# Kernel tuning notes

Hardware: AMD Instinct MI355X
Metric: run time of the kernel (lower is better)

## Reference

```python
import jax, jax.numpy as jnp
import numpy as np

C, H, W = 32, 64, 64
KH, KW = 5, 5
OH, OW = 60, 60
N_IN = C * H * W
B, S = 64, 4096
CAP = 128


def _build_indices():
    # Enumerate every (c, kh, kw, oh, ow) slot of the unfold, matching
    # fold(unfold(order)) in the torch module (stride 1, pad 0, dilation 1).
    c = np.arange(C)[:, None, None, None, None]
    kh = np.arange(KH)[None, :, None, None, None]
    kw = np.arange(KW)[None, None, :, None, None]
    oh = np.arange(OH)[None, None, None, :, None]
    ow = np.arange(OW)[None, None, None, None, :]
    ids = c * (H * W) + (oh + kh) * W + (ow + kw)          # input flat id feeding slot
    ckk = c * (KH * KW) + kh * KW + kw                     # kernel-local channel index
    j = ckk * (OH * OW) + oh * OW + ow                     # flat slot in order_convoled
    ids, j = np.broadcast_arrays(ids, j)
    ids = ids.ravel().astype(np.int64)
    j = j.ravel().astype(np.int64)
    perm = np.argsort(ids, kind='stable')
    sid, sj = ids[perm], j[perm]
    counts = np.bincount(ids, minlength=N_IN)
    Lmax = int(counts.max())                               # = 25 here
    starts = np.concatenate([[0], np.cumsum(counts)[:-1]])
    rank = np.arange(sid.shape[0]) - starts[sid]
    indices = np.full((N_IN, Lmax), -1, dtype=np.int32)
    indices[sid, rank] = sj
    return indices


def setup_inputs() -> dict:
    key = jax.random.key(0)
    spikes = jax.random.randint(key, (B, S, 1, 1), 0, N_IN, dtype=jnp.int32)
    indices = jnp.asarray(_build_indices())
    return {"spikes": spikes, "indices": indices, "out_h": OH, "out_w": OW, "cap": CAP}


def reference(spikes, indices, out_h, out_w, cap):
    Bn, Sn = spikes.shape[0], spikes.shape[1]
    L = indices.shape[1]
    nbins = out_h * out_w
    E = Sn * L                                             # events per batch element

    ids = spikes[:, :, 0, 0]                               # [B,S] flat input ids
    g = indices[ids]                                       # [B,S,L] slots, -1 padded
    valid = g >= 0
    j = jnp.where(valid, g, 0)
    bins = (j % nbins).reshape(Bn * E)                     # output bin (oh*out_w+ow)
    ckk = (j // nbins).reshape(Bn * E)                     # kernel-local index to store
    valid_f = valid.reshape(Bn * E)
    b_idx = jnp.repeat(jnp.arange(Bn, dtype=jnp.int32), E)

    # Arrival-order rank within each (batch, bin): stable sort by global bin,
    # then rank = position - segment start (running max of change points).
    gbin = jnp.where(valid_f, b_idx * nbins + bins, Bn * nbins)   # sentinel for invalid
    perm = jnp.argsort(gbin)                               # stable
    sorted_gbin = gbin[perm]
    pos = jnp.arange(Bn * E, dtype=jnp.int32)
    change = jnp.concatenate([jnp.ones((1,), bool), sorted_gbin[1:] != sorted_gbin[:-1]])
    seg_start = jax.lax.cummax(jnp.where(change, pos, 0))
    rank_sorted = pos - seg_start
    rank = jnp.zeros(Bn * E, jnp.int32).at[perm].set(rank_sorted)  # inverse perm

    # Scatter ckk into per-bin slots; invalid / overflow events go to slot=cap (dropped).
    slot = jnp.where(valid_f & (rank < cap), rank, cap)
    out = jnp.full((Bn, cap + 1, nbins), -1, dtype=spikes.dtype)
    out = out.at[b_idx, slot, bins].set(jnp.where(valid_f, ckk, -1), mode='drop')
    return out[:, :cap].reshape(Bn, cap, out_h, out_w)
```

## Files before the change

### kernel.cpp

```cpp
#include <hip/hip_runtime.h>

#define OHh   60
#define OWw   60
#define NBINS (OHh * OWw)
#define NB    64
#define NS    4096
#define CAP   128

#define NW     4
#define SEG    (NS / NW)
#define CH     (SEG / 64)
#define WSLOTS 40
#define PRE0   64

__global__ __launch_bounds__(256) void sort_spikes_row4(
    const int* __restrict__ spikes, int* __restrict__ out) {
    const int bid  = (int)blockIdx.x;
    const int b    = bid & (NB - 1);
    const int row  = bid >> 6;
    const int tid  = (int)threadIdx.x;
    const int wv   = tid >> 6;
    const int lane = tid & 63;
    const bool valid  = lane < OWw;
    const int  lane_c = valid ? lane : 127;

    __shared__ short          stage[NW][WSLOTS + 1][64];
    __shared__ unsigned short hits[NW][64];
    __shared__ int            cnt[NW][64];
    __shared__ int            ovf;

    if (tid == 0) ovf = 0;

    const int* __restrict__ sp   = spikes + b * NS + wv * SEG;
    int* __restrict__       outb = out + (size_t)b * (CAP * NBINS) + row * OWw;

    int vs[CH];
#pragma unroll
    for (int c = 0; c < CH; ++c) vs[c] = sp[c * 64 + lane];

    unsigned short* const hitbuf      = &hits[wv][0];
    short* const          stage_lane  = &stage[wv][0][lane];
    short* const          stage_dummy = &stage[wv][WSLOTS][lane];

    int count = 0;
#pragma unroll
    for (int c = 0; c < CH; ++c) {
        const int v   = vs[c];
        const int kh  = ((v >> 6) & 63) - row;
        const bool halo = (unsigned)kh < 5u;
        const int w   = v & 63;
        const int A   = (v >> 12) * 25 + kh * 5 + w;
        const unsigned short P = (unsigned short)((w << 10) | A);

        const unsigned long long mask = __ballot(halo);
        const int pos = __builtin_amdgcn_mbcnt_hi(
            (unsigned)(mask >> 32),
            __builtin_amdgcn_mbcnt_lo((unsigned)mask, 0));
        if (halo) hitbuf[pos] = P;
        const int n = __popcll(mask);

        for (int i = 0; i < n; ++i) {
            const int Pj  = (int)hitbuf[i];
            const int kw  = (Pj >> 10) - lane_c;
            const bool inwin = (unsigned)kw < 5u;
            const int val = (Pj & 0x3ff) - lane_c;
            short* a = (inwin & (count < WSLOTS))
                           ? (stage_lane + count * 64)
                           : stage_dummy;
            *a = (short)val;
            count += inwin;
        }

        if (valid) outb[(PRE0 + wv * CH + c) * NBINS + lane] = -1;
    }
    cnt[wv][lane] = count;
    if (__ballot(count > WSLOTS) && lane == 0) ovf = 1;
    __syncthreads();

    if (ovf == 0) {
        if (valid) {
            const int c0 = cnt[0][lane], c1 = cnt[1][lane];
            const int c2 = cnt[2][lane], c3 = cnt[3][lane];
            const int o1 = c0, o2 = c0 + c1, o3 = o2 + c2;
            const int total = o3 + c3;
#pragma unroll 4
            for (int i = 0; i < PRE0 / NW; ++i) {
                const int k = wv * (PRE0 / NW) + i;
                int val = -1;
                if (k < total) {
                    int wsel = 0, base = 0;
                    if (k >= o1) { wsel = 1; base = o1; }
                    if (k >= o2) { wsel = 2; base = o2; }
                    if (k >= o3) { wsel = 3; base = o3; }
                    val = (int)stage[wsel][k - base][lane];
                }
                outb[k * NBINS + lane] = val;
            }
            for (int k = PRE0 + wv; k < total && k < CAP; k += NW) {
                int wsel = 0, base = 0;
                if (k >= o1) { wsel = 1; base = o1; }
                if (k >= o2) { wsel = 2; base = o2; }
                if (k >= o3) { wsel = 3; base = o3; }
                outb[k * NBINS + lane] = (int)stage[wsel][k - base][lane];
            }
        }
    } else if (wv == 0) {
        const int* __restrict__ spf = spikes + b * NS;
        int cc = 0;
        for (int c = 0; c < NS / 64; ++c) {
            const int v = spf[c * 64 + lane];
            const int h = (v >> 6) & 63;
            unsigned long long mask = __ballot((unsigned)(h - row) < 5u);
            while (mask) {
                const int j = (int)__builtin_ctzll(mask);
                mask &= mask - 1;
                const int vj =
                    __builtin_amdgcn_readlane(v, __builtin_amdgcn_readfirstlane(j));
                const int wj  = vj & 63;
                const int khj = ((vj >> 6) & 63) - row;
                const int cj  = vj >> 12;
                const int kw  = wj - lane;
                if (((unsigned)kw < 5u) & valid) {
                    if (cc < CAP)
                        outb[cc * NBINS + lane] = cj * 25 + khj * 5 + kw;
                    ++cc;
                }
            }
        }
        if (valid)
            for (int k = cc; k < CAP; ++k) outb[k * NBINS + lane] = -1;
    }
}

extern "C" void kernel_launch(void* const* d_in, const int* in_sizes, int n_in,
                              void* d_out, int out_size, void* d_ws, size_t ws_size,
                              hipStream_t stream) {
    const int* spikes = (const int*)d_in[0];
    int* out = (int*)d_out;

    dim3 grid(OHh * NB);
    dim3 block(256);
    sort_spikes_row4<<<grid, block, 0, stream>>>(spikes, out);
}
```

Before: 147.2 us.

## Process halo hits in groups of twelve with lane-per-(hit,kw) scatter

```diff
diff --git a/kernel.cpp b/kernel.cpp
--- a/kernel.cpp
+++ b/kernel.cpp
@@ -10,8 +10,9 @@
 #define NW     4
 #define SEG    (NS / NW)
 #define CH     (SEG / 64)
-#define WSLOTS 40
+#define WSLOTS 36
 #define PRE0   64
+#define GH     12
 
 __global__ __launch_bounds__(256) void sort_spikes_row4(
     const int* __restrict__ spikes, int* __restrict__ out) {
@@ -21,15 +22,18 @@
     const int tid  = (int)threadIdx.x;
     const int wv   = tid >> 6;
     const int lane = tid & 63;
-    const bool valid  = lane < OWw;
-    const int  lane_c = valid ? lane : 127;
+    const bool valid = lane < OWw;
 
-    __shared__ short          stage[NW][WSLOTS + 1][64];
-    __shared__ unsigned short hits[NW][64];
-    __shared__ int            cnt[NW][64];
-    __shared__ int            ovf;
+    const int i_loc = lane / 5;
+    const int kw_p  = lane - 5 * i_loc;
+
+    __shared__ short        stage[NW][WSLOTS + 1][64];
+    __shared__ unsigned int hbuf[NW][64];
+    __shared__ int          cnt[NW][64];
+    __shared__ int          ovf;
 
     if (tid == 0) ovf = 0;
+    cnt[wv][lane] = 0;
 
     const int* __restrict__ sp   = spikes + b * NS + wv * SEG;
     int* __restrict__       outb = out + (size_t)b * (CAP * NBINS) + row * OWw;
@@ -38,43 +42,56 @@
 #pragma unroll
     for (int c = 0; c < CH; ++c) vs[c] = sp[c * 64 + lane];
 
-    unsigned short* const hitbuf      = &hits[wv][0];
-    short* const          stage_lane  = &stage[wv][0][lane];
-    short* const          stage_dummy = &stage[wv][WSLOTS][lane];
+    unsigned int* const hb = &hbuf[wv][0];
+    int* const          cw = &cnt[wv][0];
 
-    int count = 0;
 #pragma unroll
     for (int c = 0; c < CH; ++c) {
-        const int v   = vs[c];
-        const int kh  = ((v >> 6) & 63) - row;
+        const int v    = vs[c];
+        const int kh   = ((v >> 6) & 63) - row;
         const bool halo = (unsigned)kh < 5u;
-        const int w   = v & 63;
-        const int A   = (v >> 12) * 25 + kh * 5 + w;
-        const unsigned short P = (unsigned short)((w << 10) | A);
+        const int w    = v & 63;
+        const unsigned P = ((unsigned)w << 16) | (unsigned)((v >> 12) * 25 + kh * 5);
 
         const unsigned long long mask = __ballot(halo);
         const int pos = __builtin_amdgcn_mbcnt_hi(
             (unsigned)(mask >> 32),
             __builtin_amdgcn_mbcnt_lo((unsigned)mask, 0));
-        if (halo) hitbuf[pos] = P;
+        if (halo) hb[pos] = P;
         const int n = __popcll(mask);
 
-        for (int i = 0; i < n; ++i) {
-            const int Pj  = (int)hitbuf[i];
-            const int kw  = (Pj >> 10) - lane_c;
-            const bool inwin = (unsigned)kw < 5u;
-            const int val = (Pj & 0x3ff) - lane_c;
-            short* a = (inwin & (count < WSLOTS))
-                           ? (stage_lane + count * 64)
-                           : stage_dummy;
-            *a = (short)val;
-            count += inwin;
+        for (int g = 0; g < n; g += GH) {
+            const int  ghits = min(n - g, GH);
+            const bool pact  = i_loc < ghits;
+            const int  hidx  = pact ? (g + i_loc) : 0;
+            const unsigned Pi = hb[hidx];
+            const int wi = (int)(Pi >> 16);
+            const int Ai = (int)(Pi & 0xffffu);
+            const int ow = wi - kw_p;
+            const bool act = pact & ((unsigned)ow < (unsigned)OWw);
+
+            int rank = 0, full = 0;
+            for (int t = 0; t < ghits; ++t) {
+                const unsigned Pt = __builtin_amdgcn_readlane(Pi, 5 * t);
+                const bool cond = (unsigned)((int)(Pt >> 16) - ow) < 5u;
+                full += cond;
+                rank += (cond & (t < i_loc));
+            }
+
+            const int ow_c = act ? ow : 60;
+            const int base = cw[ow_c];
+            int slot = base + rank;
+            const bool ok = act & (slot < WSLOTS);
+            slot = ok ? slot : WSLOTS;
+            stage[wv][slot][act ? ow : lane] = (short)(Ai + kw_p);
+            cw[ow_c] = base + (act ? full : 0);
         }
 
         if (valid) outb[(PRE0 + wv * CH + c) * NBINS + lane] = -1;
     }
-    cnt[wv][lane] = count;
-    if (__ballot(count > WSLOTS) && lane == 0) ovf = 1;
+
+    const int count = cw[lane];
+    if (__ballot(valid && count > WSLOTS) && lane == 0) ovf = 1;
     __syncthreads();
 
     if (ovf == 0) {
@@ -106,6 +123,7 @@
         }
     } else if (wv == 0) {
         const int* __restrict__ spf = spikes + b * NS;
+        const int lane_c = valid ? lane : 127;
         int cc = 0;
         for (int c = 0; c < NS / 64; ++c) {
             const int v = spf[c * 64 + lane];
@@ -119,8 +137,8 @@
                 const int wj  = vj & 63;
                 const int khj = ((vj >> 6) & 63) - row;
                 const int cj  = vj >> 12;
-                const int kw  = wj - lane;
-                if (((unsigned)kw < 5u) & valid) {
+                const int kw  = wj - lane_c;
+                if ((unsigned)kw < 5u) {
                     if (cc < CAP)
                         outb[cc * NBINS + lane] = cj * 25 + khj * 5 + kw;
                     ++cc;
```

After: 151.9 us. 1.03x slower.
